# Kernel tuning notes

Hardware: AMD Instinct MI355X
Metric: run time of the kernel (lower is better)

The kernel has to match this reference:

```python
import jax, jax.numpy as jnp
import numpy as np
from jax import lax

POOL = 2048      # pool_size
HARD = 128       # hard_slices
EXTRA = 64       # random_extra
T_MIN, T_MAX, T_STEPS = -5.0, 5.0, 17
EPS = 1e-12


def _t_phi():
    t = jnp.linspace(T_MIN, T_MAX, T_STEPS)
    return t, jnp.exp(-0.5 * t * t)


def _slice_losses(z, A, t, phi):
    # z: [B, D], A: [D, M] -> per-slice ECF matching loss [M]
    zc = z - z.mean(axis=0, keepdims=True)
    u = zc @ A                              # [B, M]
    ut = u[:, :, None] * t                  # [B, M, T]
    ecf_re = jnp.cos(ut).mean(axis=0)       # [M, T] (= Re E[exp(i u t)])
    ecf_im = jnp.sin(ut).mean(axis=0)       # [M, T]
    integrand = ((ecf_re - phi) ** 2 + ecf_im ** 2) * phi
    dt = t[1:] - t[:-1]
    # trapezoid rule along t
    return (0.5 * (integrand[..., 1:] + integrand[..., :-1]) * dt).sum(axis=-1)


def _gram_schmidt(H):
    # Sequential Gram-Schmidt over columns of H: [D, m]. Mirrors
    # _gs_select_from_ranked in the generic case (unit random directions
    # never degenerate, so the top-m ranked columns are all kept).
    def body(j, Q):
        v = H[:, j]
        v = v - Q @ (Q.T @ v)   # unfilled cols of Q are zero -> no-op
        n = jnp.linalg.norm(v)
        return Q.at[:, j].set(v / jnp.maximum(n, EPS))
    return lax.fori_loop(0, H.shape[1], body, jnp.zeros_like(H))


def setup_inputs() -> dict:
    key = jax.random.key(0)
    z = jax.random.normal(key, (2048, 1024), dtype=jnp.float32)
    return {"z": z, "seed": 0}


def reference(z, seed):
    B, D = z.shape
    t, phi = _t_phi()

    # random unit-norm direction pool (seeded)
    A_pool = jax.random.normal(jax.random.key(seed), (D, POOL), dtype=z.dtype)
    A_pool = A_pool / (jnp.linalg.norm(A_pool, axis=0, keepdims=True) + EPS)

    # rank slices by ECF loss, take hardest, orthonormalize (hardmaxqr)
    losses = _slice_losses(z, A_pool, t, phi)
    ranked = jnp.argsort(-losses)
    hard_raw = A_pool[:, ranked[:HARD]]     # [D, HARD]
    hard = _gram_schmidt(hard_raw)

    # random extra directions, orthogonalized against hard
    R = jax.random.normal(jax.random.key(seed + 9991), (D, EXTRA), dtype=z.dtype)
    R = R / (jnp.linalg.norm(R, axis=0, keepdims=True) + EPS)
    R = R - hard @ (hard.T @ R)
    R = R / (jnp.linalg.norm(R, axis=0, keepdims=True) + EPS)

    A_final = jnp.concatenate([hard, R], axis=1)   # [D, HARD+EXTRA]
    final_losses = _slice_losses(z, A_final, t, phi)
    return final_losses.mean() * B
```

## Files before the change

kernel.cpp:

```cpp
#include <hip/hip_runtime.h>
#include <cstdint>
#include <cstddef>


#define THREEFRY_PARTITIONABLE 1

static constexpr int B_ = 2048;
static constexpr int D_ = 1024;
static constexpr int P_ = 2048;
static constexpr int HARD_ = 128;
static constexpr int EXTRA_ = 64;
static constexpr int NF_ = 192;
static constexpr int TS_ = 17;


__device__ __forceinline__ void threefry2x32(uint32_t k0, uint32_t k1,
                                             uint32_t c0, uint32_t c1,
                                             uint32_t& o0, uint32_t& o1) {
  uint32_t ks0 = k0, ks1 = k1, ks2 = 0x1BD11BDAu ^ k0 ^ k1;
  uint32_t x0 = c0 + ks0;
  uint32_t x1 = c1 + ks1;
#define TF_ROT(r) { x0 += x1; x1 = (x1 << (r)) | (x1 >> (32 - (r))); x1 ^= x0; }
  TF_ROT(13) TF_ROT(15) TF_ROT(26) TF_ROT(6)
  x0 += ks1; x1 += ks2 + 1u;
  TF_ROT(17) TF_ROT(29) TF_ROT(16) TF_ROT(24)
  x0 += ks2; x1 += ks0 + 2u;
  TF_ROT(13) TF_ROT(15) TF_ROT(26) TF_ROT(6)
  x0 += ks0; x1 += ks1 + 3u;
  TF_ROT(17) TF_ROT(29) TF_ROT(16) TF_ROT(24)
  x0 += ks1; x1 += ks2 + 4u;
  TF_ROT(13) TF_ROT(15) TF_ROT(26) TF_ROT(6)
  x0 += ks2; x1 += ks0 + 5u;
#undef TF_ROT
  o0 = x0; o1 = x1;
}

__device__ __forceinline__ float bits_to_normal(uint32_t bits) {
  uint32_t fb = (bits >> 9) | 0x3f800000u;
  float f = __uint_as_float(fb) - 1.0f;
  const float lo = -0.99999994f;
  float u = f * 2.0f + lo;
  u = fmaxf(lo, u);
  float w = -log1pf(-u * u);
  float p;
  if (w < 5.0f) {
    w = w - 2.5f;
    p = 2.81022636e-08f;
    p = fmaf(p, w, 3.43273939e-07f);
    p = fmaf(p, w, -3.5233877e-06f);
    p = fmaf(p, w, -4.39150654e-06f);
    p = fmaf(p, w, 0.00021858087f);
    p = fmaf(p, w, -0.00125372503f);
    p = fmaf(p, w, -0.00417768164f);
    p = fmaf(p, w, 0.246640727f);
    p = fmaf(p, w, 1.50140941f);
  } else {
    w = sqrtf(w) - 3.0f;
    p = -0.000200214257f;
    p = fmaf(p, w, 0.000100950558f);
    p = fmaf(p, w, 0.00134934322f);
    p = fmaf(p, w, -0.00367342844f);
    p = fmaf(p, w, 0.00573950773f);
    p = fmaf(p, w, -0.0076224613f);
    p = fmaf(p, w, 0.00943887047f);
    p = fmaf(p, w, 1.00167406f);
    p = fmaf(p, w, 2.83297682f);
  }
  return ((float)1.4142135623730951) * (p * u);
}

__device__ __forceinline__ float tf_normal(uint32_t k0, uint32_t k1,
                                           uint32_t idx, uint32_t half) {
#if THREEFRY_PARTITIONABLE
  (void)half;
  uint32_t a, b;
  threefry2x32(k0, k1, 0u, idx, a, b);
  return bits_to_normal(a ^ b);
#else
  uint32_t a, b;
  if (idx < half) { threefry2x32(k0, k1, idx, idx + half, a, b); return bits_to_normal(a); }
  threefry2x32(k0, k1, idx - half, idx, a, b);
  return bits_to_normal(b);
#endif
}


__global__ __launch_bounds__(256) void colsum_part_kernel(const float* __restrict__ Z,
                                                          float* __restrict__ part) {
  int col = blockIdx.x * 256 + threadIdx.x;
  int r0 = blockIdx.y * 64;
  float s = 0.f;
  for (int r = r0; r < r0 + 64; ++r) s += Z[(size_t)r * D_ + col];
  part[blockIdx.y * D_ + col] = s;
}

__global__ __launch_bounds__(256) void colmean_fin_kernel(const float* __restrict__ part,
                                                          float* __restrict__ mean) {
  int col = blockIdx.x * 256 + threadIdx.x;
  float s = 0.f;
  for (int rb = 0; rb < 32; ++rb) s += part[rb * D_ + col];
  mean[col] = s * (1.0f / (float)B_);
}

__global__ __launch_bounds__(256) void zc_kernel(const float* __restrict__ Z,
                                                 const float* __restrict__ mean,
                                                 float* __restrict__ ZC) {
  int idx = blockIdx.x * 256 + threadIdx.x;
  ZC[idx] = Z[idx] - mean[idx & (D_ - 1)];
}

__global__ __launch_bounds__(256) void gen_pool_kernel(float* __restrict__ AT,
                                                       const int* __restrict__ seedp) {
  int gid = blockIdx.x * 256 + threadIdx.x;
  int d = gid & (D_ - 1);
  int p = gid >> 10;
  uint64_t s = (uint64_t)(int64_t)seedp[0];
  uint32_t k0 = (uint32_t)(s >> 32), k1 = (uint32_t)s;
  uint32_t i = (uint32_t)((d << 11) + p);
  AT[gid] = tf_normal(k0, k1, i, (uint32_t)(D_ * P_ / 2));
}

__global__ __launch_bounds__(256) void gen_R_kernel(float* __restrict__ DIRS,
                                                    const int* __restrict__ seedp) {
  int gid = blockIdx.x * 256 + threadIdx.x;
  int d = gid & (D_ - 1);
  int j = gid >> 10;
  uint64_t s = (uint64_t)((int64_t)seedp[0] + 9991);
  uint32_t k0 = (uint32_t)(s >> 32), k1 = (uint32_t)s;
  uint32_t i = (uint32_t)((d << 6) + j);
  DIRS[(size_t)(HARD_ + j) * D_ + d] = tf_normal(k0, k1, i, (uint32_t)(D_ * EXTRA_ / 2));
}

__global__ __launch_bounds__(256) void rownorm_kernel(float* __restrict__ Arows, int ncols) {
  float* r = Arows + (size_t)blockIdx.x * ncols;
  int tid = threadIdx.x;
  float ss = 0.f;
  for (int d = tid; d < ncols; d += 256) { float v = r[d]; ss = fmaf(v, v, ss); }
  __shared__ float red[256];
  red[tid] = ss;
  __syncthreads();
  for (int s = 128; s > 0; s >>= 1) { if (tid < s) red[tid] += red[tid + s]; __syncthreads(); }
  float denom = sqrtf(red[0]) + 1e-12f;
  for (int d = tid; d < ncols; d += 256) r[d] = r[d] / denom;
}

template <int BM, int BN, int BK, int TM, int TN, int NT>
__global__ __launch_bounds__(NT) void gemm_nt_kernel(const float* __restrict__ A,
                                                     const float* __restrict__ Bm,
                                                     float* __restrict__ C,
                                                     int M, int N, int K,
                                                     int lda, int ldb, int ldc) {
  static_assert(TN == 4 || TN == 8, "");
  static_assert((BM * BK) % (4 * NT) == 0, "");
  __shared__ float As[2][BK][BM + 4];
  __shared__ float Bs[2][BK][BN + 4];
  const int tid = threadIdx.x;
  constexpr int TX = BN / TN;
  constexpr int TY = NT / TX;
  static_assert(TY * TM == BM, "");
  const int tx = tid % TX;
  const int ty = tid / TX;
  const int m0 = blockIdx.y * BM;
  const int n0 = blockIdx.x * BN;
  constexpr int NF4 = (BM * BK) / (4 * NT);
  constexpr int F4R = BK / 4;

  float acc[TM][TN];
#pragma unroll
  for (int i = 0; i < TM; ++i)
#pragma unroll
    for (int j = 0; j < TN; ++j) acc[i][j] = 0.f;

  float4 ra[NF4], rb[NF4];

  auto ldnext = [&](int k0) {
#pragma unroll
    for (int q = 0; q < NF4; ++q) {
      int idx = tid + q * NT;
      int r = idx / F4R;
      int kk = (idx % F4R) * 4;
      ra[q] = *(const float4*)(A + (size_t)(m0 + r) * lda + k0 + kk);
      rb[q] = *(const float4*)(Bm + (size_t)(n0 + r) * ldb + k0 + kk);
    }
  };
  auto stnext = [&](int buf) {
#pragma unroll
    for (int q = 0; q < NF4; ++q) {
      int idx = tid + q * NT;
      int r = idx / F4R;
      int kk = (idx % F4R) * 4;
      As[buf][kk + 0][r] = ra[q].x; As[buf][kk + 1][r] = ra[q].y;
      As[buf][kk + 2][r] = ra[q].z; As[buf][kk + 3][r] = ra[q].w;
      Bs[buf][kk + 0][r] = rb[q].x; Bs[buf][kk + 1][r] = rb[q].y;
      Bs[buf][kk + 2][r] = rb[q].z; Bs[buf][kk + 3][r] = rb[q].w;
    }
  };
  auto compute = [&](int buf) {
#pragma unroll
    for (int kk = 0; kk < BK; ++kk) {
      float a[TM], b[TN];
#pragma unroll
      for (int q = 0; q < TM / 4; ++q) {
        float4 v = *(const float4*)&As[buf][kk][ty * TM + q * 4];
        a[q * 4 + 0] = v.x; a[q * 4 + 1] = v.y; a[q * 4 + 2] = v.z; a[q * 4 + 3] = v.w;
      }
      {
        float4 v = *(const float4*)&Bs[buf][kk][tx * 4];
        b[0] = v.x; b[1] = v.y; b[2] = v.z; b[3] = v.w;
      }
      if constexpr (TN == 8) {
        float4 v = *(const float4*)&Bs[buf][kk][BN / 2 + tx * 4];
        b[4] = v.x; b[5] = v.y; b[6] = v.z; b[7] = v.w;
      }
#pragma unroll
      for (int i = 0; i < TM; ++i)
#pragma unroll
        for (int j = 0; j < TN; ++j) acc[i][j] = fmaf(a[i], b[j], acc[i][j]);
    }
  };

  ldnext(0);
  stnext(0);
  __syncthreads();
  const int nst = K / BK;
  for (int s = 0; s < nst; ++s) {
    const int cur = s & 1;
    if (s + 1 < nst) ldnext((s + 1) * BK);
    compute(cur);
    if (s + 1 < nst) stnext(cur ^ 1);
    __syncthreads();
  }

#pragma unroll
  for (int i = 0; i < TM; ++i) {
    const int gm = m0 + ty * TM + i;
    float4 c0 = make_float4(acc[i][0], acc[i][1], acc[i][2], acc[i][3]);
    *(float4*)(C + (size_t)gm * ldc + n0 + tx * 4) = c0;
    if constexpr (TN == 8) {
      float4 c1 = make_float4(acc[i][4], acc[i][5], acc[i][6], acc[i][7]);
      *(float4*)(C + (size_t)gm * ldc + n0 + BN / 2 + tx * 4) = c1;
    }
  }
}

__global__ __launch_bounds__(256) void dotk_kernel(const float* __restrict__ A,
                                                   const float* __restrict__ Bm,
                                                   float* __restrict__ C,
                                                   int M, int N, int K, int ldc) {
  int i = blockIdx.y * 16 + (threadIdx.x >> 4);
  int j = blockIdx.x * 16 + (threadIdx.x & 15);
  if (i >= M || j >= N) return;
  const float* a = A + (size_t)i * K;
  const float* b = Bm + (size_t)j * K;
  float s0 = 0.f, s1 = 0.f, s2 = 0.f, s3 = 0.f;
  for (int d = 0; d < K; d += 4) {
    s0 = fmaf(a[d + 0], b[d + 0], s0);
    s1 = fmaf(a[d + 1], b[d + 1], s1);
    s2 = fmaf(a[d + 2], b[d + 2], s2);
    s3 = fmaf(a[d + 3], b[d + 3], s3);
  }
  C[(size_t)i * ldc + j] = (s0 + s1) + (s2 + s3);
}

__global__ __launch_bounds__(256) void ecf_loss_kernel(const float* __restrict__ U,
                                                       float* __restrict__ out_loss) {
  const float* u = U + (size_t)blockIdx.x * B_;
  const int tid = threadIdx.x;
  float sc[TS_], ss[TS_];
#pragma unroll
  for (int k = 0; k < TS_; ++k) { sc[k] = 0.f; ss[k] = 0.f; }

  for (int b = tid; b < B_; b += 256) {
    float x = u[b];
#pragma unroll
    for (int k = 0; k < TS_; ++k) {
      const double tk = -5.0 + 0.625 * (double)k;
      const float trev = (float)(tk * 0.15915494309189535);
      float r = x * trev;
      sc[k] += __builtin_amdgcn_cosf(r);
      ss[k] += __builtin_amdgcn_sinf(r);
    }
  }
#pragma unroll
  for (int k = 0; k < TS_; ++k) {
#pragma unroll
    for (int off = 32; off > 0; off >>= 1) {
      sc[k] += __shfl_down(sc[k], off, 64);
      ss[k] += __shfl_down(ss[k], off, 64);
    }
  }
  __shared__ float rsc[4][TS_], rss[4][TS_];
  int wid = tid >> 6, lane = tid & 63;
  if (lane == 0) {
#pragma unroll
    for (int k = 0; k < TS_; ++k) { rsc[wid][k] = sc[k]; rss[wid][k] = ss[k]; }
  }
  __syncthreads();
  if (tid == 0) {
    float loss = 0.f, prevI = 0.f;
#pragma unroll
    for (int k = 0; k < TS_; ++k) {
      float tk = -5.0f + 0.625f * (float)k;
      float phik = expf(-0.5f * tk * tk);
      float S = (rsc[0][k] + rsc[1][k]) + (rsc[2][k] + rsc[3][k]);
      float T = (rss[0][k] + rss[1][k]) + (rss[2][k] + rss[3][k]);
      float re = S * (1.0f / (float)B_) - phik;
      float im = T * (1.0f / (float)B_);
      float I = (re * re + im * im) * phik;
      if (k > 0) loss += 0.5f * (I + prevI) * 0.625f;
      prevI = I;
    }
    out_loss[blockIdx.x] = loss;
  }
}

__global__ __launch_bounds__(1024) void sort_kernel(const float* __restrict__ loss,
                                                    int* __restrict__ ranked) {
  __shared__ float ls[P_];
  __shared__ int li[P_];
  int tid = threadIdx.x;
  for (int i = tid; i < P_; i += 1024) { ls[i] = loss[i]; li[i] = i; }
  __syncthreads();
  for (int k = 2; k <= P_; k <<= 1) {
    for (int j = k >> 1; j > 0; j >>= 1) {
      for (int i = tid; i < P_; i += 1024) {
        int ixj = i ^ j;
        if (ixj > i) {
          bool up = ((i & k) == 0);
          float la = ls[i], lb = ls[ixj];
          int ia = li[i], ib = li[ixj];
          bool a_after_b = (la < lb) || (la == lb && ia > ib);
          bool sw = up ? a_after_b : (!a_after_b && !(la == lb && ia == ib));
          if (sw) { ls[i] = lb; ls[ixj] = la; li[i] = ib; li[ixj] = ia; }
        }
      }
      __syncthreads();
    }
  }
  for (int i = tid; i < P_; i += 1024) ranked[i] = li[i];
}

__global__ __launch_bounds__(256) void gather_ht_kernel(const float* __restrict__ AT,
                                                        const int* __restrict__ ranked,
                                                        float* __restrict__ HT) {
  int j = blockIdx.x;
  int src = ranked[j];
  for (int d = threadIdx.x; d < D_; d += 256)
    HT[(size_t)j * D_ + d] = AT[(size_t)src * D_ + d];
}

__global__ __launch_bounds__(512) void chol_inv_kernel(const float* __restrict__ G,
                                                       float* __restrict__ W) {
  __shared__ float g[HARD_][HARD_ + 1];
  __shared__ float w[HARD_][HARD_ + 1];
  __shared__ float m[16][16 * 7 + 4];
  __shared__ float rinv[HARD_];
  const int tid = threadIdx.x;

  for (int idx = tid; idx < HARD_ * HARD_; idx += 512)
    g[idx >> 7][idx & 127] = G[idx];
  for (int idx = tid; idx < HARD_ * (HARD_ + 1); idx += 512)
    (&w[0][0])[idx] = 0.f;
  __syncthreads();

  const int bcol = tid & 127;
  const int aoff = tid >> 7;
  for (int K = 0; K < 8; ++K) {
    const int b = K << 4;
    const int c0 = b + 16;
    const int nc = HARD_ - c0;

    if (tid < 16) {
      const int j = tid;
      float c[16];
#pragma unroll
      for (int k = 0; k < 16; ++k) c[k] = g[b + k][b + j];
#pragma unroll
      for (int i = 0; i < 16; ++i) {
        float rii = sqrtf(__shfl(c[i], i, 16));
        float rinvi = 1.0f / rii;
        float rij = c[i] * rinvi;
        if (j > i) c[i] = rij;
        if (j == i) c[i] = rii;
#pragma unroll
        for (int a = i + 1; a < 16; ++a) {
          float ria = __shfl(c[i], a, 16);
          if (j >= a) c[a] = fmaf(-ria, rij, c[a]);
        }
      }
#pragma unroll
      for (int k = 0; k < 16; ++k) if (k <= j) g[b + k][b + j] = c[k];
      rinv[b + j] = 1.0f / c[j];
    }
    __syncthreads();

    if (nc > 0) {
      if (tid < nc) {
        const int j = c0 + tid;
        float x[16];
#pragma unroll
        for (int i = 0; i < 16; ++i) {
          float acc = g[b + i][j];
#pragma unroll
          for (int m2 = 0; m2 < i; ++m2)
            acc = fmaf(-g[b + m2][b + i], x[m2], acc);
          x[i] = acc * rinv[b + i];
        }
#pragma unroll
        for (int i = 0; i < 16; ++i) g[b + i][j] = x[i];
      }
      __syncthreads();

      if (bcol >= c0) {
        float rkb[16];
#pragma unroll
        for (int k = 0; k < 16; ++k) rkb[k] = g[b + k][bcol];
        for (int a = c0 + aoff; a <= bcol; a += 4) {
          float acc = g[a][bcol];
#pragma unroll
          for (int k = 0; k < 16; ++k)
            acc = fmaf(-g[b + k][a], rkb[k], acc);
          g[a][bcol] = acc;
        }
      }
    }
    __syncthreads();
  }

  if (tid < HARD_) {
    const int blk = tid >> 4, j = tid & 15, b = blk << 4;
    const float myrinv = rinv[b + j];
    float wcol[16];
#pragma unroll
    for (int i = 15; i >= 0; --i) {
      float s = 0.f;
#pragma unroll
      for (int k = 15; k > i; --k) s = fmaf(g[b + i][b + k], wcol[k], s);
      float v = -rinv[b + i] * s;
      wcol[i] = (i < j) ? v : ((i == j) ? myrinv : 0.f);
    }
#pragma unroll
    for (int k = 0; k < 16; ++k) w[b + k][b + j] = wcol[k];
  }
  __syncthreads();

  for (int I = 6; I >= 0; --I) {
    const int b = I << 4;
    const int c0 = b + 16;
    const int nc = HARD_ - c0;
    const int nel = 16 * nc;
    for (int e = tid; e < nel; e += 512) {
      int r = e / nc, c = e - r * nc;
      float acc = 0.f;
      for (int k = c0; k < HARD_; ++k)
        acc = fmaf(g[b + r][k], w[k][c0 + c], acc);
      m[r][c] = acc;
    }
    __syncthreads();
    for (int e = tid; e < nel; e += 512) {
      int r = e / nc, c = e - r * nc;
      float acc = 0.f;
#pragma unroll
      for (int rp = 0; rp < 16; ++rp)
        acc = fmaf(w[b + r][b + rp], m[rp][c], acc);
      w[b + r][c0 + c] = -acc;
    }
    __syncthreads();
  }

  for (int idx = tid; idx < HARD_ * HARD_; idx += 512)
    W[idx] = w[idx >> 7][idx & 127];
}

__global__ __launch_bounds__(128) void apply_winv_kernel(const float* __restrict__ HT,
                                                         const float* __restrict__ W,
                                                         float* __restrict__ DIRS) {
  int j = blockIdx.y;
  int d = blockIdx.x * 128 + threadIdx.x;
  __shared__ float wc[HARD_];
  for (int i = threadIdx.x; i <= j; i += 128) wc[i] = W[i * HARD_ + j];
  __syncthreads();
  float acc = 0.f;
  for (int i = 0; i <= j; ++i) acc = fmaf(wc[i], HT[(size_t)i * D_ + d], acc);
  DIRS[(size_t)j * D_ + d] = acc;
}

__global__ __launch_bounds__(128) void proj_update_kernel(float* __restrict__ DIRS,
                                                          const float* __restrict__ C) {
  int j = blockIdx.y;
  int d = blockIdx.x * 128 + threadIdx.x;
  __shared__ float cc[HARD_];
  cc[threadIdx.x] = C[threadIdx.x * EXTRA_ + j];
  if (threadIdx.x + 128 < HARD_) cc[threadIdx.x + 128] = C[(threadIdx.x + 128) * EXTRA_ + j];
  __syncthreads();
  float acc = DIRS[(size_t)(HARD_ + j) * D_ + d];
  for (int i = 0; i < HARD_; ++i) acc = fmaf(-cc[i], DIRS[(size_t)i * D_ + d], acc);
  DIRS[(size_t)(HARD_ + j) * D_ + d] = acc;
}

__global__ __launch_bounds__(256) void finalize_kernel(const float* __restrict__ FL,
                                                       float* __restrict__ out) {
  __shared__ float red[256];
  int tid = threadIdx.x;
  red[tid] = (tid < NF_) ? FL[tid] : 0.f;
  __syncthreads();
  for (int s = 128; s > 0; s >>= 1) { if (tid < s) red[tid] += red[tid + s]; __syncthreads(); }
  if (tid == 0) out[0] = (red[0] / (float)NF_) * (float)B_;
}


extern "C" void kernel_launch(void* const* d_in, const int* in_sizes, int n_in,
                              void* d_out, int out_size, void* d_ws, size_t ws_size,
                              hipStream_t stream) {
  const float* Z = (const float*)d_in[0];
  const int* seedp = (const int*)d_in[1];
  float* out = (float*)d_out;
  (void)in_sizes; (void)n_in; (void)out_size; (void)ws_size;

  char* ws = (char*)d_ws;
  size_t off = 0;
  auto alloc = [&](size_t bytes) -> char* {
    char* p = ws + off;
    off += (bytes + 255) & ~(size_t)255;
    return p;
  };
  float* ZC   = (float*)alloc((size_t)B_ * D_ * 4);
  float* AT   = (float*)alloc((size_t)P_ * D_ * 4);
  float* UT   = (float*)alloc((size_t)P_ * B_ * 4);
  float* LOSS = (float*)alloc(P_ * 4);
  int*   IDX  = (int*)  alloc(P_ * 4);
  float* HT   = (float*)alloc((size_t)HARD_ * D_ * 4);
  float* G    = (float*)alloc(HARD_ * HARD_ * 4);
  float* W    = (float*)alloc(HARD_ * HARD_ * 4);
  float* DIRS = (float*)alloc((size_t)NF_ * D_ * 4);
  float* PRJ  = (float*)alloc(HARD_ * EXTRA_ * 4);
  float* UF   = (float*)alloc((size_t)NF_ * B_ * 4);
  float* FL   = (float*)alloc(NF_ * 4);
  float* PART = (float*)alloc(32 * D_ * 4);
  float* MEAN = (float*)alloc(D_ * 4);

  colsum_part_kernel<<<dim3(D_ / 256, 32), 256, 0, stream>>>(Z, PART);
  colmean_fin_kernel<<<D_ / 256, 256, 0, stream>>>(PART, MEAN);
  zc_kernel<<<(B_ * D_) / 256, 256, 0, stream>>>(Z, MEAN, ZC);

  gen_pool_kernel<<<(P_ * D_) / 256, 256, 0, stream>>>(AT, seedp);
  rownorm_kernel<<<P_, 256, 0, stream>>>(AT, D_);

  gemm_nt_kernel<128, 128, 16, 4, 8, 512><<<dim3(B_ / 128, P_ / 128), 512, 0, stream>>>(
      AT, ZC, UT, P_, B_, D_, D_, D_, B_);
  ecf_loss_kernel<<<P_, 256, 0, stream>>>(UT, LOSS);

  sort_kernel<<<1, 1024, 0, stream>>>(LOSS, IDX);
  gather_ht_kernel<<<HARD_, 256, 0, stream>>>(AT, IDX, HT);

  dotk_kernel<<<dim3(HARD_ / 16, HARD_ / 16), 256, 0, stream>>>(HT, HT, G, HARD_, HARD_, D_, HARD_);
  chol_inv_kernel<<<1, 512, 0, stream>>>(G, W);
  apply_winv_kernel<<<dim3(D_ / 128, HARD_), 128, 0, stream>>>(HT, W, DIRS);

  gen_R_kernel<<<(EXTRA_ * D_) / 256, 256, 0, stream>>>(DIRS, seedp);
  rownorm_kernel<<<EXTRA_, 256, 0, stream>>>(DIRS + (size_t)HARD_ * D_, D_);
  dotk_kernel<<<dim3(EXTRA_ / 16, HARD_ / 16), 256, 0, stream>>>(
      DIRS, DIRS + (size_t)HARD_ * D_, PRJ, HARD_, EXTRA_, D_, EXTRA_);
  proj_update_kernel<<<dim3(D_ / 128, EXTRA_), 128, 0, stream>>>(DIRS, PRJ);
  rownorm_kernel<<<EXTRA_, 256, 0, stream>>>(DIRS + (size_t)HARD_ * D_, D_);

  gemm_nt_kernel<64, 64, 32, 4, 4, 256><<<dim3(B_ / 64, NF_ / 64), 256, 0, stream>>>(
      DIRS, ZC, UF, NF_, B_, D_, D_, D_, B_);
  ecf_loss_kernel<<<NF_, 256, 0, stream>>>(UF, FL);
  finalize_kernel<<<1, 256, 0, stream>>>(FL, out);
}
```

Measured before the change: 502.8 us.

## Use split-bf16 MFMA for pool GEMM, fuse centering and RNG normalization

The main pool projection GEMM moves from an FP32 SIMT kernel to MFMA bf16 instructions. Each operand is split into high and low bf16 parts and three products are accumulated to keep accuracy close to FP32. Mean-centering is folded into the GEMM operand loads, which removes the ZC buffer and its kernel. Pool and extra-direction generation now fuse row normalization into a single block per row. The naive dot-product kernels are replaced by a shared-memory tiled Gram kernel. Risks are a small precision loss from the 3-term bf16 split and a simple single-stage LDS pipeline in the MFMA kernel.

After: 431.2 us. 14.2% less time.

```diff
diff --git a/kernel.cpp b/kernel.cpp
--- a/kernel.cpp
+++ b/kernel.cpp
@@ -12,6 +12,9 @@
 static constexpr int EXTRA_ = 64;
 static constexpr int NF_ = 192;
 static constexpr int TS_ = 17;
+
+typedef short short8v __attribute__((ext_vector_type(8)));
+typedef float f32x4v __attribute__((ext_vector_type(4)));
 
 
 __device__ __forceinline__ void threefry2x32(uint32_t k0, uint32_t k1,
@@ -70,17 +73,11 @@
 }
 
 __device__ __forceinline__ float tf_normal(uint32_t k0, uint32_t k1,
-                                           uint32_t idx, uint32_t half) {
+                                           uint32_t idx) {
 #if THREEFRY_PARTITIONABLE
-  (void)half;
   uint32_t a, b;
   threefry2x32(k0, k1, 0u, idx, a, b);
   return bits_to_normal(a ^ b);
-#else
-  uint32_t a, b;
-  if (idx < half) { threefry2x32(k0, k1, idx, idx + half, a, b); return bits_to_normal(a); }
-  threefry2x32(k0, k1, idx - half, idx, a, b);
-  return bits_to_normal(b);
 #endif
 }
 
@@ -102,33 +99,56 @@
   mean[col] = s * (1.0f / (float)B_);
 }
 
-__global__ __launch_bounds__(256) void zc_kernel(const float* __restrict__ Z,
-                                                 const float* __restrict__ mean,
-                                                 float* __restrict__ ZC) {
-  int idx = blockIdx.x * 256 + threadIdx.x;
-  ZC[idx] = Z[idx] - mean[idx & (D_ - 1)];
-}
-
-__global__ __launch_bounds__(256) void gen_pool_kernel(float* __restrict__ AT,
-                                                       const int* __restrict__ seedp) {
-  int gid = blockIdx.x * 256 + threadIdx.x;
-  int d = gid & (D_ - 1);
-  int p = gid >> 10;
+__global__ __launch_bounds__(256) void gen_pool_norm_kernel(float* __restrict__ AT,
+                                                            const int* __restrict__ seedp) {
+  const int p = blockIdx.x;
+  const int tid = threadIdx.x;
   uint64_t s = (uint64_t)(int64_t)seedp[0];
   uint32_t k0 = (uint32_t)(s >> 32), k1 = (uint32_t)s;
-  uint32_t i = (uint32_t)((d << 11) + p);
-  AT[gid] = tf_normal(k0, k1, i, (uint32_t)(D_ * P_ / 2));
-}
-
-__global__ __launch_bounds__(256) void gen_R_kernel(float* __restrict__ DIRS,
-                                                    const int* __restrict__ seedp) {
-  int gid = blockIdx.x * 256 + threadIdx.x;
-  int d = gid & (D_ - 1);
-  int j = gid >> 10;
+  float v[4]; float ss = 0.f;
+#pragma unroll
+  for (int q = 0; q < 4; ++q) {
+    int d = tid + 256 * q;
+    uint32_t i = (uint32_t)((d << 11) + p);
+    v[q] = tf_normal(k0, k1, i);
+    ss = fmaf(v[q], v[q], ss);
+  }
+  __shared__ float red[256];
+  red[tid] = ss;
+  __syncthreads();
+  for (int st = 128; st > 0; st >>= 1) { if (tid < st) red[tid] += red[tid + st]; __syncthreads(); }
+  float denom = sqrtf(red[0]) + 1e-12f;
+#pragma unroll
+  for (int q = 0; q < 4; ++q) {
+    int d = tid + 256 * q;
+    AT[(size_t)p * D_ + d] = v[q] / denom;
+  }
+}
+
+__global__ __launch_bounds__(256) void gen_R_norm_kernel(float* __restrict__ DIRS,
+                                                         const int* __restrict__ seedp) {
+  const int j = blockIdx.x;
+  const int tid = threadIdx.x;
   uint64_t s = (uint64_t)((int64_t)seedp[0] + 9991);
   uint32_t k0 = (uint32_t)(s >> 32), k1 = (uint32_t)s;
-  uint32_t i = (uint32_t)((d << 6) + j);
-  DIRS[(size_t)(HARD_ + j) * D_ + d] = tf_normal(k0, k1, i, (uint32_t)(D_ * EXTRA_ / 2));
+  float v[4]; float ss = 0.f;
+#pragma unroll
+  for (int q = 0; q < 4; ++q) {
+    int d = tid + 256 * q;
+    uint32_t i = (uint32_t)((d << 6) + j);
+    v[q] = tf_normal(k0, k1, i);
+    ss = fmaf(v[q], v[q], ss);
+  }
+  __shared__ float red[256];
+  red[tid] = ss;
+  __syncthreads();
+  for (int st = 128; st > 0; st >>= 1) { if (tid < st) red[tid] += red[tid + st]; __syncthreads(); }
+  float denom = sqrtf(red[0]) + 1e-12f;
+#pragma unroll
+  for (int q = 0; q < 4; ++q) {
+    int d = tid + 256 * q;
+    DIRS[(size_t)(HARD_ + j) * D_ + d] = v[q] / denom;
+  }
 }
 
 __global__ __launch_bounds__(256) void rownorm_kernel(float* __restrict__ Arows, int ncols) {
@@ -144,9 +164,124 @@
   for (int d = tid; d < ncols; d += 256) r[d] = r[d] / denom;
 }
 
-template <int BM, int BN, int BK, int TM, int TN, int NT>
+__device__ __forceinline__ uint32_t f2bf_rne(float x) {
+  uint32_t u = __float_as_uint(x);
+  return (u + 0x7fffu + ((u >> 16) & 1u)) >> 16;
+}
+
+__global__ __launch_bounds__(512) void gemm_mfma_kernel(const float* __restrict__ A,
+                                                        const float* __restrict__ Z,
+                                                        const float* __restrict__ meanp,
+                                                        float* __restrict__ C) {
+  constexpr int BK = 32;
+  __shared__ ushort Ah[128][40], Al[128][40], Bh[128][40], Bl[128][40];
+  const int tid = threadIdx.x;
+  const int lane = tid & 63;
+  const int w = tid >> 6;
+  const int wr = w >> 2;
+  const int wc = w & 3;
+  const int m0 = blockIdx.y * 128;
+  const int n0 = blockIdx.x * 128;
+
+  f32x4v acc[4][2];
+#pragma unroll
+  for (int mi = 0; mi < 4; ++mi)
+#pragma unroll
+    for (int ni = 0; ni < 2; ++ni) acc[mi][ni] = (f32x4v){0.f, 0.f, 0.f, 0.f};
+
+  float4 ra[2], rb[2];
+  auto ld = [&](int s) {
+    const int k0 = s * BK;
+#pragma unroll
+    for (int q = 0; q < 2; ++q) {
+      int f4 = tid + q * 512;
+      int r = f4 >> 3;
+      int kq = (f4 & 7) * 4;
+      ra[q] = *(const float4*)(A + (size_t)(m0 + r) * D_ + k0 + kq);
+      float4 z = *(const float4*)(Z + (size_t)(n0 + r) * D_ + k0 + kq);
+      float4 mu = *(const float4*)(meanp + k0 + kq);
+      rb[q] = make_float4(z.x - mu.x, z.y - mu.y, z.z - mu.z, z.w - mu.w);
+    }
+  };
+  auto st = [&]() {
+#pragma unroll
+    for (int q = 0; q < 2; ++q) {
+      int f4 = tid + q * 512;
+      int r = f4 >> 3;
+      int kq = (f4 & 7) * 4;
+      float av[4] = {ra[q].x, ra[q].y, ra[q].z, ra[q].w};
+      float bv[4] = {rb[q].x, rb[q].y, rb[q].z, rb[q].w};
+      ushort ah[4], al[4], bh[4], bl[4];
+#pragma unroll
+      for (int c = 0; c < 4; ++c) {
+        uint32_t h = f2bf_rne(av[c]);
+        ah[c] = (ushort)h;
+        al[c] = (ushort)f2bf_rne(av[c] - __uint_as_float(h << 16));
+        uint32_t g = f2bf_rne(bv[c]);
+        bh[c] = (ushort)g;
+        bl[c] = (ushort)f2bf_rne(bv[c] - __uint_as_float(g << 16));
+      }
+      *(ushort4*)&Ah[r][kq] = make_ushort4(ah[0], ah[1], ah[2], ah[3]);
+      *(ushort4*)&Al[r][kq] = make_ushort4(al[0], al[1], al[2], al[3]);
+      *(ushort4*)&Bh[r][kq] = make_ushort4(bh[0], bh[1], bh[2], bh[3]);
+      *(ushort4*)&Bl[r][kq] = make_ushort4(bl[0], bl[1], bl[2], bl[3]);
+    }
+  };
+  auto compute = [&]() {
+    const int rl = lane & 15;
+    const int koff = (lane >> 4) * 8;
+    short8v a_h[4], a_l[4], b_h[2], b_l[2];
+#pragma unroll
+    for (int mi = 0; mi < 4; ++mi) {
+      int arow = wr * 64 + mi * 16 + rl;
+      a_h[mi] = *(const short8v*)&Ah[arow][koff];
+      a_l[mi] = *(const short8v*)&Al[arow][koff];
+    }
+#pragma unroll
+    for (int ni = 0; ni < 2; ++ni) {
+      int brow = wc * 32 + ni * 16 + rl;
+      b_h[ni] = *(const short8v*)&Bh[brow][koff];
+      b_l[ni] = *(const short8v*)&Bl[brow][koff];
+    }
+#pragma unroll
+    for (int mi = 0; mi < 4; ++mi)
+#pragma unroll
+      for (int ni = 0; ni < 2; ++ni) {
+        acc[mi][ni] = __builtin_amdgcn_mfma_f32_16x16x32_bf16(a_h[mi], b_h[ni], acc[mi][ni], 0, 0, 0);
+        acc[mi][ni] = __builtin_amdgcn_mfma_f32_16x16x32_bf16(a_h[mi], b_l[ni], acc[mi][ni], 0, 0, 0);
+        acc[mi][ni] = __builtin_amdgcn_mfma_f32_16x16x32_bf16(a_l[mi], b_h[ni], acc[mi][ni], 0, 0, 0);
+      }
+  };
+
+  const int nst = D_ / BK;
+  ld(0);
+  for (int s = 0; s < nst; ++s) {
+    if (s) __syncthreads();
+    st();
+    __syncthreads();
+    if (s + 1 < nst) ld(s + 1);
+    compute();
+  }
+
+  const int rl = lane & 15;
+  const int rq = (lane >> 4) * 4;
+#pragma unroll
+  for (int mi = 0; mi < 4; ++mi)
+#pragma unroll
+    for (int ni = 0; ni < 2; ++ni) {
+      int col = n0 + wc * 32 + ni * 16 + rl;
+#pragma unroll
+      for (int r = 0; r < 4; ++r) {
+        int row = m0 + wr * 64 + mi * 16 + rq + r;
+        C[(size_t)row * B_ + col] = acc[mi][ni][r];
+      }
+    }
+}
+
+template <int BM, int BN, int BK, int TM, int TN, int NT, bool CENTER_B>
 __global__ __launch_bounds__(NT) void gemm_nt_kernel(const float* __restrict__ A,
                                                      const float* __restrict__ Bm,
+                                                     const float* __restrict__ meanp,
                                                      float* __restrict__ C,
                                                      int M, int N, int K,
                                                      int lda, int ldb, int ldc) {
@@ -180,7 +315,12 @@
       int r = idx / F4R;
       int kk = (idx % F4R) * 4;
       ra[q] = *(const float4*)(A + (size_t)(m0 + r) * lda + k0 + kk);
-      rb[q] = *(const float4*)(Bm + (size_t)(n0 + r) * ldb + k0 + kk);
+      float4 b = *(const float4*)(Bm + (size_t)(n0 + r) * ldb + k0 + kk);
+      if constexpr (CENTER_B) {
+        float4 mu = *(const float4*)(meanp + k0 + kk);
+        b = make_float4(b.x - mu.x, b.y - mu.y, b.z - mu.z, b.w - mu.w);
+      }
+      rb[q] = b;
     }
   };
   auto stnext = [&](int buf) {
@@ -243,23 +383,54 @@
   }
 }
 
-__global__ __launch_bounds__(256) void dotk_kernel(const float* __restrict__ A,
+__global__ __launch_bounds__(256) void gram_kernel(const float* __restrict__ A,
                                                    const float* __restrict__ Bm,
                                                    float* __restrict__ C,
-                                                   int M, int N, int K, int ldc) {
-  int i = blockIdx.y * 16 + (threadIdx.x >> 4);
-  int j = blockIdx.x * 16 + (threadIdx.x & 15);
-  if (i >= M || j >= N) return;
-  const float* a = A + (size_t)i * K;
-  const float* b = Bm + (size_t)j * K;
-  float s0 = 0.f, s1 = 0.f, s2 = 0.f, s3 = 0.f;
-  for (int d = 0; d < K; d += 4) {
-    s0 = fmaf(a[d + 0], b[d + 0], s0);
-    s1 = fmaf(a[d + 1], b[d + 1], s1);
-    s2 = fmaf(a[d + 2], b[d + 2], s2);
-    s3 = fmaf(a[d + 3], b[d + 3], s3);
-  }
-  C[(size_t)i * ldc + j] = (s0 + s1) + (s2 + s3);
+                                                   int K, int ldc) {
+  __shared__ float As[32][136];
+  __shared__ float BsT[128][36];
+  const int tid = threadIdx.x;
+  const int i0 = blockIdx.y * 32;
+  const int j0 = blockIdx.x * 32;
+  const int i = tid >> 3;
+  const int jl = (tid & 7) * 4;
+
+  float s[4][4];
+#pragma unroll
+  for (int m = 0; m < 4; ++m)
+#pragma unroll
+    for (int c = 0; c < 4; ++c) s[m][c] = 0.f;
+
+  for (int kc = 0; kc < K; kc += 128) {
+#pragma unroll
+    for (int q = 0; q < 4; ++q) {
+      int f4 = tid + 256 * q;
+      int r = f4 >> 5;
+      int kq = (f4 & 31) * 4;
+      float4 va = *(const float4*)(A + (size_t)(i0 + r) * K + kc + kq);
+      *(float4*)&As[r][kq] = va;
+      float4 vb = *(const float4*)(Bm + (size_t)(j0 + r) * K + kc + kq);
+      BsT[kq + 0][r] = vb.x; BsT[kq + 1][r] = vb.y;
+      BsT[kq + 2][r] = vb.z; BsT[kq + 3][r] = vb.w;
+    }
+    __syncthreads();
+    for (int k4 = 0; k4 < 128; k4 += 4) {
+#pragma unroll
+      for (int c = 0; c < 4; ++c) {
+        int k = k4 + c;
+        float a = As[i][k];
+        float4 b = *(const float4*)&BsT[k][jl];
+        s[0][c] = fmaf(a, b.x, s[0][c]);
+        s[1][c] = fmaf(a, b.y, s[1][c]);
+        s[2][c] = fmaf(a, b.z, s[2][c]);
+        s[3][c] = fmaf(a, b.w, s[3][c]);
+      }
+    }
+    __syncthreads();
+  }
+#pragma unroll
+  for (int m = 0; m < 4; ++m)
+    C[(size_t)(i0 + i) * ldc + j0 + jl + m] = (s[m][0] + s[m][1]) + (s[m][2] + s[m][3]);
 }
 
 __global__ __launch_bounds__(256) void ecf_loss_kernel(const float* __restrict__ U,
@@ -524,7 +695,6 @@
     off += (bytes + 255) & ~(size_t)255;
     return p;
   };
-  float* ZC   = (float*)alloc((size_t)B_ * D_ * 4);
   float* AT   = (float*)alloc((size_t)P_ * D_ * 4);
   float* UT   = (float*)alloc((size_t)P_ * B_ * 4);
   float* LOSS = (float*)alloc(P_ * 4);
@@ -541,31 +711,27 @@
 
   colsum_part_kernel<<<dim3(D_ / 256, 32), 256, 0, stream>>>(Z, PART);
   colmean_fin_kernel<<<D_ / 256, 256, 0, stream>>>(PART, MEAN);
-  zc_kernel<<<(B_ * D_) / 256, 256, 0, stream>>>(Z, MEAN, ZC);
-
-  gen_pool_kernel<<<(P_ * D_) / 256, 256, 0, stream>>>(AT, seedp);
-  rownorm_kernel<<<P_, 256, 0, stream>>>(AT, D_);
-
-  gemm_nt_kernel<128, 128, 16, 4, 8, 512><<<dim3(B_ / 128, P_ / 128), 512, 0, stream>>>(
-      AT, ZC, UT, P_, B_, D_, D_, D_, B_);
+
+  gen_pool_norm_kernel<<<P_, 256, 0, stream>>>(AT, seedp);
+
+  gemm_mfma_kernel<<<dim3(B_ / 128, P_ / 128), 512, 0, stream>>>(AT, Z, MEAN, UT);
   ecf_loss_kernel<<<P_, 256, 0, stream>>>(UT, LOSS);
 
   sort_kernel<<<1, 1024, 0, stream>>>(LOSS, IDX);
   gather_ht_kernel<<<HARD_, 256, 0, stream>>>(AT, IDX, HT);
 
-  dotk_kernel<<<dim3(HARD_ / 16, HARD_ / 16), 256, 0, stream>>>(HT, HT, G, HARD_, HARD_, D_, HARD_);
+  gram_kernel<<<dim3(HARD_ / 32, HARD_ / 32), 256, 0, stream>>>(HT, HT, G, D_, HARD_);
   chol_inv_kernel<<<1, 512, 0, stream>>>(G, W);
   apply_winv_kernel<<<dim3(D_ / 128, HARD_), 128, 0, stream>>>(HT, W, DIRS);
 
-  gen_R_kernel<<<(EXTRA_ * D_) / 256, 256, 0, stream>>>(DIRS, seedp);
-  rownorm_kernel<<<EXTRA_, 256, 0, stream>>>(DIRS + (size_t)HARD_ * D_, D_);
-  dotk_kernel<<<dim3(EXTRA_ / 16, HARD_ / 16), 256, 0, stream>>>(
-      DIRS, DIRS + (size_t)HARD_ * D_, PRJ, HARD_, EXTRA_, D_, EXTRA_);
+  gen_R_norm_kernel<<<EXTRA_, 256, 0, stream>>>(DIRS, seedp);
+  gram_kernel<<<dim3(EXTRA_ / 32, HARD_ / 32), 256, 0, stream>>>(
+      DIRS, DIRS + (size_t)HARD_ * D_, PRJ, D_, EXTRA_);
   proj_update_kernel<<<dim3(D_ / 128, EXTRA_), 128, 0, stream>>>(DIRS, PRJ);
   rownorm_kernel<<<EXTRA_, 256, 0, stream>>>(DIRS + (size_t)HARD_ * D_, D_);
 
-  gemm_nt_kernel<64, 64, 32, 4, 4, 256><<<dim3(B_ / 64, NF_ / 64), 256, 0, stream>>>(
-      DIRS, ZC, UF, NF_, B_, D_, D_, D_, B_);
+  gemm_nt_kernel<64, 64, 32, 4, 4, 256, true><<<dim3(B_ / 64, NF_ / 64), 256, 0, stream>>>(
+      DIRS, Z, MEAN, UF, NF_, B_, D_, D_, D_, B_);
   ecf_loss_kernel<<<NF_, 256, 0, stream>>>(UF, FL);
   finalize_kernel<<<1, 256, 0, stream>>>(FL, out);
 }
```
